# Performance work log

Hardware: AMD Instinct MI355X
Metric: run time of the kernel (lower is better)

The kernel has to match this reference:

```python
import jax, jax.numpy as jnp
import numpy as np

V = 50257
H = 1032          # hidden_size + 8
IN = 2 * H        # gru input size
S = 8192          # encoder seq len


def setup_inputs() -> dict:
    key = jax.random.key(0)
    ks = jax.random.split(key, 12)
    s = 0.02
    return {
        "word_input": jax.random.randint(ks[0], (1,), 0, V),
        "last_context": jax.random.normal(ks[1], (1, 1, H), jnp.float32),
        "prev_hidden": jax.random.normal(ks[2], (1, 1, H), jnp.float32),
        "encoder_outputs": jax.random.normal(ks[3], (S, 1, H), jnp.float32),
        "emb": jax.random.normal(ks[4], (V, H), jnp.float32) * s,
        "W_ih": jax.random.normal(ks[5], (3 * H, IN), jnp.float32) * s,
        "W_hh": jax.random.normal(ks[6], (3 * H, H), jnp.float32) * s,
        "b_ih": jnp.zeros((3 * H,), jnp.float32),
        "b_hh": jnp.zeros((3 * H,), jnp.float32),
        "W_a": jax.random.normal(ks[7], (H, H), jnp.float32) * s,
        "b_a": jnp.zeros((H,), jnp.float32),
        "W_out": jax.random.normal(ks[8], (V, 2 * H), jnp.float32) * s,
        "b_out": jnp.zeros((V,), jnp.float32),
    }


def reference(word_input, last_context, prev_hidden, encoder_outputs,
              emb, W_ih, W_hh, b_ih, b_hh, W_a, b_a, W_out, b_out):
    # --- embedding + concat with last context -> GRU input [1, 2H]
    embedded = emb[word_input].reshape(1, H)            # dropout = identity (eval)
    x = jnp.concatenate([embedded, last_context[0]], axis=1)   # [1, 2H]
    h = prev_hidden[0]                                  # [1, H]

    # --- single-step GRU (PyTorch gate layout: r, z, n)
    gx = x @ W_ih.T + b_ih                              # [1, 3H]
    gh = h @ W_hh.T + b_hh                              # [1, 3H]
    xr, xz, xn = jnp.split(gx, 3, axis=1)
    hr, hz, hn = jnp.split(gh, 3, axis=1)
    r = jax.nn.sigmoid(xr + hr)
    z = jax.nn.sigmoid(xz + hz)
    n = jnp.tanh(xn + r * hn)
    h_new = (1.0 - z) * n + z * h                       # [1, H]

    # --- Luong attention over all encoder steps in one batched matmul
    enc = encoder_outputs[:, 0, :]                      # [S, H]
    proj = enc @ W_a.T + b_a                            # [S, H]
    scores = proj @ h_new[0]                            # [S]
    attn_weights = jax.nn.softmax(scores)               # [S]
    attn_context = (attn_weights[:, None] * enc).sum(axis=0, keepdims=True)  # [1, H]

    # --- output projection + log softmax
    joined = jnp.concatenate([h_new, attn_context], axis=1)    # [1, 2H]
    output = jax.nn.log_softmax(joined @ W_out.T + b_out, axis=1)  # [1, V]

    current_hidden = h_new[None]                        # [1, 1, H]
    attn_w = attn_weights[None, None]                   # [1, 1, S]
    return output, attn_context[None], current_hidden, attn_w
```

## Files before the change

kernel.cpp:

```cpp
#include <hip/hip_runtime.h>
#include <math.h>

#define V  50257
#define H  1032
#define INW 2064
#define S  8192

#define O_CTX  50257
#define O_HID  51289
#define O_ATTN 52321

#define OFF_GXP  0
#define OFF_GHP  6192
#define OFF_HNEW 12384
#define OFF_V    13416
#define OFF_CTXV 14448
#define OFF_SC   15480
#define OFF_PART 23672

#define GRU_B   1548
#define VA_B    80
#define NPART   2048

__device__ __forceinline__ float waveReduceSum(float v) {
#pragma unroll
  for (int off = 32; off > 0; off >>= 1) v += __shfl_down(v, off);
  return v;
}

__device__ __forceinline__ float dot4(const float4 a, const float4 b) {
  return a.x * b.x + a.y * b.y + a.z * b.z + a.w * b.w;
}

__global__ __launch_bounds__(256) void gru_mv_kernel(
    const int* __restrict__ word, const float* __restrict__ emb,
    const float* __restrict__ lc, const float* __restrict__ ph,
    const float* __restrict__ W_ih, const float* __restrict__ W_hh,
    float* __restrict__ ws) {
  __shared__ __align__(16) float xh[INW + H];
  float* gxp = ws + OFF_GXP;
  float* ghp = ws + OFF_GHP;
  int t = threadIdx.x, wv = t >> 6, lane = t & 63, b = blockIdx.x;
  if (b == 0) for (int i = t; i < H; i += 256) (ws + OFF_V)[i] = 0.f;
  if (b == 1) for (int i = t; i < H; i += 256) (ws + OFF_CTXV)[i] = 0.f;
  int w0 = word[0];
  for (int i = t; i < INW; i += 256) xh[i] = (i < H) ? emb[(size_t)w0 * H + i] : lc[i - H];
  for (int i = t; i < H; i += 256) xh[INW + i] = ph[i];
  __syncthreads();
  int g = b * 4 + wv;
  int j = g >> 1, c = g & 1;
  const float4* wi = (const float4*)(W_ih + (size_t)j * INW + c * (INW / 2));
  const float4* x4 = (const float4*)(xh + c * (INW / 2));
  float a0 = 0.f;
  for (int i = lane; i < INW / 8; i += 64) a0 += dot4(wi[i], x4[i]);
  const float4* wh = (const float4*)(W_hh + (size_t)j * H + c * (H / 2));
  const float4* h4 = (const float4*)(xh + INW + c * (H / 2));
  float a1 = 0.f;
  for (int i = lane; i < H / 8; i += 64) a1 += dot4(wh[i], h4[i]);
  a0 = waveReduceSum(a0); a1 = waveReduceSum(a1);
  if (lane == 0) { gxp[c * 3096 + j] = a0; ghp[c * 3096 + j] = a1; }
}

__device__ __forceinline__ float gru_elem(
    const float* __restrict__ gxp, const float* __restrict__ ghp,
    const float* __restrict__ b_ih, const float* __restrict__ b_hh,
    const float* __restrict__ ph, int k) {
  float gxr = gxp[k] + gxp[3096 + k],           ghr = ghp[k] + ghp[3096 + k];
  float gxz = gxp[H + k] + gxp[3096 + H + k],   ghz = ghp[H + k] + ghp[3096 + H + k];
  float gxn = gxp[2 * H + k] + gxp[3096 + 2 * H + k];
  float ghn = ghp[2 * H + k] + ghp[3096 + 2 * H + k];
  float r = 1.f / (1.f + expf(-(gxr + ghr + b_ih[k] + b_hh[k])));
  float z = 1.f / (1.f + expf(-(gxz + ghz + b_ih[H + k] + b_hh[H + k])));
  float n = tanhf(gxn + b_ih[2 * H + k] + r * (ghn + b_hh[2 * H + k]));
  return (1.f - z) * n + z * ph[k];
}

__global__ __launch_bounds__(256) void vafin_kernel(
    const float* __restrict__ W_a, const float* __restrict__ ph,
    const float* __restrict__ b_ih, const float* __restrict__ b_hh,
    float* __restrict__ ws, float* __restrict__ out) {
  __shared__ float hsh[65];
  const float* gxp = ws + OFF_GXP;
  const float* ghp = ws + OFF_GHP;
  int b = blockIdx.x, t = threadIdx.x;
  if (b < VA_B) {
    int ct = b % 5, jc = b / 5;
    int j0 = jc * 65;
    int nj = min(65, H - j0);
    if (t < nj) hsh[t] = gru_elem(gxp, ghp, b_ih, b_hh, ph, j0 + t);
    __syncthreads();
    int k = ct * 256 + t;
    if (k < H) {
      float acc = 0.f;
      for (int j = 0; j < nj; ++j) acc += W_a[(size_t)(j0 + j) * H + k] * hsh[j];
      atomicAdd(ws + OFF_V + k, acc);
    }
  } else {
    int base = (b - VA_B) * 258;
    for (int kk = t; kk < 258; kk += 256) {
      int k = base + kk;
      float hv = gru_elem(gxp, ghp, b_ih, b_hh, ph, k);
      (ws + OFF_HNEW)[k] = hv;
      out[O_HID + k] = hv;
    }
  }
}

__global__ __launch_bounds__(256) void scores_kernel(
    const float* __restrict__ enc, float* __restrict__ ws) {
  int t = threadIdx.x, wv = t >> 6, lane = t & 63;
  int s = blockIdx.x * 4 + wv;
  const float4* row = (const float4*)(enc + (size_t)s * H);
  const float4* v4  = (const float4*)(ws + OFF_V);
  float acc = 0.f;
  for (int i = lane; i < H / 4; i += 64) acc += dot4(row[i], v4[i]);
  acc = waveReduceSum(acc);
  if (lane == 0) (ws + OFF_SC)[s] = acc;
}

__global__ __launch_bounds__(256) void ctx_kernel(
    const float* __restrict__ enc, float* __restrict__ ws,
    float* __restrict__ out) {
  __shared__ float red[256];
  __shared__ float wsh[64];
  const float* sc = ws + OFF_SC;
  int t = threadIdx.x, b = blockIdx.x;
  float m = -3.4e38f;
  for (int i = t; i < S; i += 256) m = fmaxf(m, sc[i]);
  red[t] = m; __syncthreads();
  for (int off = 128; off; off >>= 1) {
    if (t < off) red[t] = fmaxf(red[t], red[t + off]);
    __syncthreads();
  }
  m = red[0]; __syncthreads();
  float s = 0.f;
  for (int i = t; i < S; i += 256) s += expf(sc[i] - m);
  red[t] = s; __syncthreads();
  for (int off = 128; off; off >>= 1) {
    if (t < off) red[t] += red[t + off];
    __syncthreads();
  }
  float inv = 1.f / red[0];
  int ct = b % 5, yc = b / 5;
  int s0 = yc * 64;
  if (t < 64) wsh[t] = expf(sc[s0 + t] - m) * inv;
  __syncthreads();
  if (ct == 0 && t < 64) out[O_ATTN + s0 + t] = wsh[t];
  int k = ct * 256 + t;
  if (k < H) {
    float acc = 0.f;
    for (int si = 0; si < 64; ++si) acc += wsh[si] * enc[(size_t)(s0 + si) * H + k];
    atomicAdd(ws + OFF_CTXV + k, acc);
  }
}

__global__ __launch_bounds__(256) void logits_kernel(
    const float* __restrict__ W_out, const float* __restrict__ b_out,
    float* __restrict__ ws, float* __restrict__ out) {
  __shared__ __align__(16) float joined[INW];
  __shared__ float pm[4], psv[4];
  int t = threadIdx.x, wv = t >> 6, lane = t & 63;
  for (int k = t; k < H; k += 256) {
    joined[k]     = (ws + OFF_HNEW)[k];
    joined[H + k] = (ws + OFF_CTXV)[k];
  }
  __syncthreads();
  if (blockIdx.x == 0) {
    for (int k = t; k < H; k += 256) out[O_CTX + k] = joined[H + k];
  }
  const float4* j4 = (const float4*)joined;
  int gw = blockIdx.x * 4 + wv;
  float lm = -3.4e38f, ls = 0.f;
  for (int r = gw; r < V; r += NPART * 4) {
    const float4* row = (const float4*)(W_out + (size_t)r * INW);
    float acc = 0.f;
    for (int i = lane; i < INW / 4; i += 64) acc += dot4(row[i], j4[i]);
    acc = waveReduceSum(acc);
    if (lane == 0) {
      float x = acc + b_out[r];
      out[r] = x;
      float nm = fmaxf(lm, x);
      ls = ls * expf(lm - nm) + expf(x - nm);
      lm = nm;
    }
  }
  if (lane == 0) { pm[wv] = lm; psv[wv] = ls; }
  __syncthreads();
  if (t == 0) {
    float m = pm[0], sb = psv[0];
    for (int q = 1; q < 4; ++q) {
      float nm = fmaxf(m, pm[q]);
      sb = sb * expf(m - nm) + psv[q] * expf(pm[q] - nm);
      m = nm;
    }
    (ws + OFF_PART)[2 * blockIdx.x]     = m;
    (ws + OFF_PART)[2 * blockIdx.x + 1] = sb;
  }
}

__global__ __launch_bounds__(256) void apply_kernel(
    float* __restrict__ out, const float* __restrict__ ws) {
  __shared__ float mm[256], ssv[256];
  const float* partials = ws + OFF_PART;
  int t = threadIdx.x;
  float m = -3.4e38f, s = 0.f;
  for (int i = t; i < NPART; i += 256) {
    float bm = partials[2 * i], bs = partials[2 * i + 1];
    float nm = fmaxf(m, bm);
    s = s * expf(m - nm) + bs * expf(bm - nm);
    m = nm;
  }
  mm[t] = m; ssv[t] = s; __syncthreads();
  for (int off = 128; off; off >>= 1) {
    if (t < off) {
      float m2 = mm[t + off], s2 = ssv[t + off];
      float nm = fmaxf(mm[t], m2);
      ssv[t] = ssv[t] * expf(mm[t] - nm) + s2 * expf(m2 - nm);
      mm[t] = nm;
    }
    __syncthreads();
  }
  float L = mm[0] + logf(ssv[0]);
  int i = blockIdx.x * 256 + t;
  if (i < V) out[i] -= L;
}

extern "C" void kernel_launch(void* const* d_in, const int* in_sizes, int n_in,
                              void* d_out, int out_size, void* d_ws, size_t ws_size,
                              hipStream_t stream) {
  const int*   word  = (const int*)d_in[0];
  const float* lc    = (const float*)d_in[1];
  const float* ph    = (const float*)d_in[2];
  const float* enc   = (const float*)d_in[3];
  const float* emb   = (const float*)d_in[4];
  const float* W_ih  = (const float*)d_in[5];
  const float* W_hh  = (const float*)d_in[6];
  const float* b_ih  = (const float*)d_in[7];
  const float* b_hh  = (const float*)d_in[8];
  const float* W_a   = (const float*)d_in[9];
  const float* W_out = (const float*)d_in[11];
  const float* b_out = (const float*)d_in[12];
  float* out = (float*)d_out;
  float* ws  = (float*)d_ws;

  gru_mv_kernel<<<GRU_B, 256, 0, stream>>>(word, emb, lc, ph, W_ih, W_hh, ws);
  vafin_kernel<<<VA_B + 4, 256, 0, stream>>>(W_a, ph, b_ih, b_hh, ws, out);
  scores_kernel<<<2048, 256, 0, stream>>>(enc, ws);
  ctx_kernel<<<640, 256, 0, stream>>>(enc, ws, out);
  logits_kernel<<<NPART, 256, 0, stream>>>(W_out, b_out, ws, out);
  apply_kernel<<<(V + 255) / 256, 256, 0, stream>>>(out, ws);
}
```

Before: 143.5 us.

## Fuse softmax partials into scores kernel and process two rows per wave

The scores kernel now has each wave compute two encoder rows and emit per-block online-softmax (max, sum) partials. The context kernel then reduces 1024 partials instead of scanning all 8192 scores twice in each of its 640 blocks. The logits kernel also handles two W_out rows per wave, sharing the joined-vector load, to raise memory-level parallelism. The cost is fewer scores blocks and a clamped duplicate row read at the tail.

```diff
diff --git a/kernel.cpp b/kernel.cpp
--- a/kernel.cpp
+++ b/kernel.cpp
@@ -16,10 +16,12 @@
 #define OFF_V    13416
 #define OFF_CTXV 14448
 #define OFF_SC   15480
-#define OFF_PART 23672
+#define OFF_SCP  23672
+#define OFF_PART 25720
 
 #define GRU_B   1548
 #define VA_B    80
+#define SC_B    1024
 #define NPART   2048
 
 __device__ __forceinline__ float waveReduceSum(float v) {
@@ -108,42 +110,69 @@
 
 __global__ __launch_bounds__(256) void scores_kernel(
     const float* __restrict__ enc, float* __restrict__ ws) {
+  __shared__ float wm[4], wsv[4];
   int t = threadIdx.x, wv = t >> 6, lane = t & 63;
-  int s = blockIdx.x * 4 + wv;
-  const float4* row = (const float4*)(enc + (size_t)s * H);
-  const float4* v4  = (const float4*)(ws + OFF_V);
-  float acc = 0.f;
-  for (int i = lane; i < H / 4; i += 64) acc += dot4(row[i], v4[i]);
-  acc = waveReduceSum(acc);
-  if (lane == 0) (ws + OFF_SC)[s] = acc;
+  int s0 = blockIdx.x * 8 + wv * 2;
+  const float4* R0 = (const float4*)(enc + (size_t)s0 * H);
+  const float4* R1 = (const float4*)(enc + (size_t)(s0 + 1) * H);
+  const float4* v4 = (const float4*)(ws + OFF_V);
+  float a0 = 0.f, a1 = 0.f;
+  for (int i = lane; i < H / 4; i += 64) {
+    float4 c = v4[i];
+    a0 += dot4(R0[i], c);
+    a1 += dot4(R1[i], c);
+  }
+  a0 = waveReduceSum(a0); a1 = waveReduceSum(a1);
+  if (lane == 0) {
+    (ws + OFF_SC)[s0]     = a0;
+    (ws + OFF_SC)[s0 + 1] = a1;
+    float m = fmaxf(a0, a1);
+    wm[wv] = m;
+    wsv[wv] = expf(a0 - m) + expf(a1 - m);
+  }
+  __syncthreads();
+  if (t == 0) {
+    float m = wm[0], s = wsv[0];
+    for (int q = 1; q < 4; ++q) {
+      float nm = fmaxf(m, wm[q]);
+      s = s * expf(m - nm) + wsv[q] * expf(wm[q] - nm);
+      m = nm;
+    }
+    (ws + OFF_SCP)[2 * blockIdx.x]     = m;
+    (ws + OFF_SCP)[2 * blockIdx.x + 1] = s;
+  }
 }
 
 __global__ __launch_bounds__(256) void ctx_kernel(
     const float* __restrict__ enc, float* __restrict__ ws,
     float* __restrict__ out) {
-  __shared__ float red[256];
+  __shared__ float rm[256], rs[256];
   __shared__ float wsh[64];
-  const float* sc = ws + OFF_SC;
+  const float* scp = ws + OFF_SCP;
+  const float* sc  = ws + OFF_SC;
   int t = threadIdx.x, b = blockIdx.x;
-  float m = -3.4e38f;
-  for (int i = t; i < S; i += 256) m = fmaxf(m, sc[i]);
-  red[t] = m; __syncthreads();
+  float m = -3.4e38f, s = 0.f;
+  for (int i = t; i < SC_B; i += 256) {
+    float bm = scp[2 * i], bs = scp[2 * i + 1];
+    float nm = fmaxf(m, bm);
+    s = s * expf(m - nm) + bs * expf(bm - nm);
+    m = nm;
+  }
+  rm[t] = m; rs[t] = s; __syncthreads();
   for (int off = 128; off; off >>= 1) {
-    if (t < off) red[t] = fmaxf(red[t], red[t + off]);
+    if (t < off) {
+      float m2 = rm[t + off], s2 = rs[t + off];
+      float nm = fmaxf(rm[t], m2);
+      rs[t] = rs[t] * expf(rm[t] - nm) + s2 * expf(m2 - nm);
+      rm[t] = nm;
+    }
     __syncthreads();
   }
-  m = red[0]; __syncthreads();
-  float s = 0.f;
-  for (int i = t; i < S; i += 256) s += expf(sc[i] - m);
-  red[t] = s; __syncthreads();
-  for (int off = 128; off; off >>= 1) {
-    if (t < off) red[t] += red[t + off];
-    __syncthreads();
-  }
-  float inv = 1.f / red[0];
+  float M = rm[0];
+  float inv = 1.f / rs[0];
   int ct = b % 5, yc = b / 5;
   int s0 = yc * 64;
-  if (t < 64) wsh[t] = expf(sc[s0 + t] - m) * inv;
+  if (t < 64) wsh[t] = expf(sc[s0 + t] - M) * inv;
   __syncthreads();
   if (ct == 0 && t < 64) out[O_ATTN + s0 + t] = wsh[t];
   int k = ct * 256 + t;
@@ -171,17 +200,30 @@
   const float4* j4 = (const float4*)joined;
   int gw = blockIdx.x * 4 + wv;
   float lm = -3.4e38f, ls = 0.f;
-  for (int r = gw; r < V; r += NPART * 4) {
-    const float4* row = (const float4*)(W_out + (size_t)r * INW);
-    float acc = 0.f;
-    for (int i = lane; i < INW / 4; i += 64) acc += dot4(row[i], j4[i]);
-    acc = waveReduceSum(acc);
+  for (int r0 = gw * 2; r0 < V; r0 += 2 * NPART * 4) {
+    int r1 = min(r0 + 1, V - 1);
+    const float4* R0 = (const float4*)(W_out + (size_t)r0 * INW);
+    const float4* R1 = (const float4*)(W_out + (size_t)r1 * INW);
+    float a0 = 0.f, a1 = 0.f;
+    for (int i = lane; i < INW / 4; i += 64) {
+      float4 c = j4[i];
+      a0 += dot4(R0[i], c);
+      a1 += dot4(R1[i], c);
+    }
+    a0 = waveReduceSum(a0); a1 = waveReduceSum(a1);
     if (lane == 0) {
-      float x = acc + b_out[r];
-      out[r] = x;
-      float nm = fmaxf(lm, x);
-      ls = ls * expf(lm - nm) + expf(x - nm);
+      float x0 = a0 + b_out[r0];
+      out[r0] = x0;
+      float nm = fmaxf(lm, x0);
+      ls = ls * expf(lm - nm) + expf(x0 - nm);
       lm = nm;
+      if (r0 + 1 < V) {
+        float x1 = a1 + b_out[r1];
+        out[r1] = x1;
+        nm = fmaxf(lm, x1);
+        ls = ls * expf(lm - nm) + expf(x1 - nm);
+        lm = nm;
+      }
     }
   }
   if (lane == 0) { pm[wv] = lm; psv[wv] = ls; }
@@ -245,7 +287,7 @@
 
   gru_mv_kernel<<<GRU_B, 256, 0, stream>>>(word, emb, lc, ph, W_ih, W_hh, ws);
   vafin_kernel<<<VA_B + 4, 256, 0, stream>>>(W_a, ph, b_ih, b_hh, ws, out);
-  scores_kernel<<<2048, 256, 0, stream>>>(enc, ws);
+  scores_kernel<<<SC_B, 256, 0, stream>>>(enc, ws);
   ctx_kernel<<<640, 256, 0, stream>>>(enc, ws, out);
   logits_kernel<<<NPART, 256, 0, stream>>>(W_out, b_out, ws, out);
   apply_kernel<<<(V + 255) / 256, 256, 0, stream>>>(out, ws);
```

Result: faster. 140.1 us (-2.4%).
